# Optimization experiments

Measured on AMD Instinct MI355X. Metric: run time of the kernel, lower is better.

## Reference

```python
import jax, jax.numpy as jnp
import numpy as np

# SLAYER neuron / simulation parameters (from network.yaml)
THETA = 10.0      # spike threshold
TAU_SR = 10.0     # SRM (psp) kernel time constant
TAU_REF = 1.0     # refractory kernel time constant
SCALE_REF = 2.0   # refractory scale (kernel = -scaleRef*theta*alpha(t))
TS = 1.0          # simulation step (ms)
TK = 100          # FIR truncation length for the psp kernel (tauSr=10 -> fully decayed)

B, NIN, NHID, NOUT, T = 32, 2312, 512, 10, 350

# discrete refractory kernel ref[n] = C_REF * n * D_REF**n  (alpha shape)
D_REF = float(np.exp(-TS / TAU_REF))
C_REF = float(-SCALE_REF * THETA * np.e * TS / TAU_REF)


def srm_kernel():
    # eps(t) = (t/tauSr) * exp(1 - t/tauSr), peak value 1 at t = tauSr
    t = jnp.arange(TK, dtype=jnp.float32) * TS
    return (t / TAU_SR) * jnp.exp(1.0 - t / TAU_SR)


def psp(x):
    """Causal FIR filter along time. x: [B, C, T] -> [B, C, T]."""
    b, c, t = x.shape
    k = srm_kernel()[::-1].reshape(1, 1, TK)  # lax.conv correlates, so flip
    xp = jnp.pad(x.reshape(b * c, 1, t), ((0, 0), (0, 0), (TK - 1, 0)))
    y = jax.lax.conv_general_dilated(xp, k, (1,), 'VALID')
    return y.reshape(b, c, t)


def dense(W, x):
    # 1x1 conv over channels, applied at every time step
    return jnp.einsum('oi,bit->bot', W, x)


@jax.custom_vjp
def spike_fn(u):
    return (u >= THETA).astype(u.dtype)

def _spike_fwd(u):
    return spike_fn(u), u

def _spike_bwd(u, g):
    # SLAYER surrogate gradient: rho(u) = scaleRho * exp(-|u - theta| / tauRho)
    return (g * jnp.exp(-jnp.abs(u - THETA) / 1.0),)

spike_fn.defvjp(_spike_fwd, _spike_bwd)


def spike_layer(u_in):
    """Threshold-and-refractory spike dynamics via a 2-state IIR realization of
    the alpha refractory kernel. u_in: [B, C, T] -> spikes [B, C, T]."""
    uT = jnp.moveaxis(u_in, -1, 0)  # [T, B, C]
    zero = jnp.zeros(uT.shape[1:], uT.dtype)

    def step(carry, u_t):
        a, b = carry  # a = conv(spikes, D^n), b = conv(spikes, n*D^n)
        u = u_t + C_REF * b          # membrane = psp drive + refractory
        s = spike_fn(u)
        a_new = D_REF * a + s
        b_new = D_REF * b + D_REF * a
        return (a_new, b_new), s

    _, sT = jax.lax.scan(step, (zero, zero), uT)
    return jnp.moveaxis(sT, 0, -1)


def setup_inputs() -> dict:
    key = jax.random.key(0)
    k1, k2, k3 = jax.random.split(key, 3)
    spikeInput = (jax.random.uniform(k1, (B, NIN, T)) < 0.05).astype(jnp.float32)
    W1 = jax.random.normal(k2, (NHID, NIN), dtype=jnp.float32) * 0.05
    W2 = jax.random.normal(k3, (NOUT, NHID), dtype=jnp.float32) * 0.05
    return {"spikeInput": spikeInput, "W1": W1, "W2": W2}


def reference(spikeInput, W1, W2):
    s1 = spike_layer(dense(W1, psp(spikeInput)))
    s2 = spike_layer(dense(W2, psp(s1)))
    return s2
```

## Files before the change

kernel.cpp:

```cpp
#include <hip/hip_runtime.h>
#include <stdint.h>

#define B_SZ   32
#define NIN    2312
#define NHID   512
#define NOUT   10
#define T_SZ   350
#define NW32   73
#define NW64   8
#define NHALF  256
#define NROW   2313

#define DS_D   0.9048374180359595
#define CS_D   0.2718281828459045
#define D100_D 4.5399929762484854e-05
#define DREF_F 0.36787944117144233f
#define CREF_F -54.36563656918091f

#define NCHUNK 7
#define CLEN   50
#define NPF    10

__global__ __launch_bounds__(384) void k12(const float* __restrict__ x,
                                           const float* __restrict__ W1,
                                           uint32_t* __restrict__ bits1,
                                           float* __restrict__ W1s) {
    __shared__ float lds[32 * T_SZ];
    const int bid = blockIdx.x;
    const int tid = threadIdx.x;
    if (bid < NW32 * B_SZ) {
        const int w = bid % NW32;
        const int b = bid / NW32;
        const int rows = (NIN - (w << 5) < 32) ? (NIN - (w << 5)) : 32;
        const float* base = x + ((size_t)(b * NIN + (w << 5))) * T_SZ;
        const int nf4 = (rows * T_SZ) >> 2;
        for (int f = tid; f < nf4; f += 384)
            ((float4*)lds)[f] = ((const float4*)base)[f];
        __syncthreads();
        if (tid < T_SZ) {
            uint32_t bits = 0;
            for (int j = 0; j < rows; ++j)
                bits |= (lds[j * T_SZ + tid] > 0.5f) ? (1u << j) : 0u;
            bits1[(size_t)(b * T_SZ + tid) * NW32 + w] = bits;
        }
    } else if (bid < NW32 * B_SZ + NW32 * 16) {
        float (*tile)[33] = (float (*)[33])lds;
        const int bb = bid - NW32 * B_SZ;
        const int i0 = (bb % NW32) * 32, o0 = (bb / NW32) * 32;
        const int tx = tid & 31, ty = tid >> 5;
#pragma unroll
        for (int r = 0; r < 3; ++r) {
            int row = ty + 12 * r;
            if (row < 32) {
                int o = o0 + row, i = i0 + tx;
                if (i < NIN) tile[row][tx] = W1[(size_t)o * NIN + i];
            }
        }
        __syncthreads();
#pragma unroll
        for (int r = 0; r < 3; ++r) {
            int row = ty + 12 * r;
            if (row < 32) {
                int i = i0 + row, o = o0 + tx;
                if (i < NIN)
                    W1s[((size_t)(o >> 8) * NROW + i) * NHALF + (o & 255)] = tile[tx][row];
            }
        }
    } else {
        if (tid < NHALF) {
            W1s[((size_t)0 * NROW + NIN) * NHALF + tid] = 0.0f;
            W1s[((size_t)1 * NROW + NIN) * NHALF + tid] = 0.0f;
        }
    }
}

__global__ __launch_bounds__(256) void k3_dense1(const uint32_t* __restrict__ bits1,
                                                 const float* __restrict__ W1s,
                                                 float* __restrict__ z1ct) {
    __shared__ uint32_t words[128];
    __shared__ uint16_t pfx[80];
    __shared__ uint16_t idxbuf[NIN + 16];
    __shared__ float red[3][NHALF];
    __shared__ float fin[NHALF];

    const int id = blockIdx.x;
    const int h = (id >> 2) & 1;
    const int bt = ((id >> 3) << 2) | (id & 3);
    const int tid = threadIdx.x;
    const int wv = tid >> 6, lane = tid & 63;

    if (tid < 128) words[tid] = (tid < NW32) ? bits1[(size_t)bt * NW32 + tid] : 0u;
    __syncthreads();

    if (wv == 0) {
        uint32_t w0 = words[lane];
        uint32_t w1 = words[lane + 64];
        int p0 = __popc(w0), p1 = __popc(w1);
        int s0 = p0, s1 = p1;
#pragma unroll
        for (int off = 1; off < 64; off <<= 1) {
            int u0 = __shfl_up(s0, off);
            int u1 = __shfl_up(s1, off);
            if (lane >= off) { s0 += u0; s1 += u1; }
        }
        int tot0 = __shfl(s0, 63);
        pfx[lane] = (uint16_t)(s0 - p0);
        if (lane < 9) pfx[lane + 64] = (uint16_t)(tot0 + s1 - p1);
        if (lane == 8) pfx[73] = (uint16_t)(tot0 + s1);
    }
    __syncthreads();

    const int ntot = pfx[73];
    const int npad = (ntot + 15) & ~15;
    if (tid < NW32) {
        uint32_t m = words[tid];
        int p = pfx[tid];
        while (m) {
            int j = __builtin_ctz(m);
            m &= m - 1;
            idxbuf[p++] = (uint16_t)((tid << 5) + j);
        }
    }
    if (tid >= 240) {
        int k = tid - 240;
        if (ntot + k < npad) idxbuf[ntot + k] = (uint16_t)NIN;
    }
    __syncthreads();

    const float* Wh = W1s + (size_t)h * NROW * NHALF;
    float4 acc = make_float4(0.f, 0.f, 0.f, 0.f);
    for (int r = wv; r < npad; r += 16) {
        int i0 = idxbuf[r], i1 = idxbuf[r + 4], i2 = idxbuf[r + 8], i3 = idxbuf[r + 12];
        float4 v0 = ((const float4*)(Wh + (size_t)i0 * NHALF))[lane];
        float4 v1 = ((const float4*)(Wh + (size_t)i1 * NHALF))[lane];
        float4 v2 = ((const float4*)(Wh + (size_t)i2 * NHALF))[lane];
        float4 v3 = ((const float4*)(Wh + (size_t)i3 * NHALF))[lane];
        acc.x += v0.x; acc.y += v0.y; acc.z += v0.z; acc.w += v0.w;
        acc.x += v1.x; acc.y += v1.y; acc.z += v1.z; acc.w += v1.w;
        acc.x += v2.x; acc.y += v2.y; acc.z += v2.z; acc.w += v2.w;
        acc.x += v3.x; acc.y += v3.y; acc.z += v3.z; acc.w += v3.w;
    }
    if (wv > 0) ((float4*)red[wv - 1])[lane] = acc;
    __syncthreads();
    if (wv == 0) {
        float4 a1 = ((float4*)red[0])[lane];
        float4 a2 = ((float4*)red[1])[lane];
        float4 a3 = ((float4*)red[2])[lane];
        acc.x = ((acc.x + a1.x) + a2.x) + a3.x;
        acc.y = ((acc.y + a1.y) + a2.y) + a3.y;
        acc.z = ((acc.z + a1.z) + a2.z) + a3.z;
        acc.w = ((acc.w + a1.w) + a2.w) + a3.w;
        ((float4*)fin)[lane] = acc;
    }
    __syncthreads();
    const int och = (h << 8) + tid;
    const int oc = och >> 6, l6 = och & 63;
    const int b = bt / T_SZ, t = bt - b * T_SZ;
    z1ct[((size_t)(b * NW64 + oc) * T_SZ + t) * 64 + l6] = fin[tid];
}

__global__ __launch_bounds__(512) void k45(const float* __restrict__ z1ct,
                                           const float* __restrict__ W2,
                                           float* __restrict__ z2ct) {
    __shared__ float W2s[NHID * NOUT];
    __shared__ uint64_t sw[CLEN][NW64];
    const int tid = threadIdx.x;
    const int wv = tid >> 6, lane = tid & 63;
    const int b = blockIdx.x / NCHUNK;
    const int ck = blockIdx.x % NCHUNK;
    const int tstart = ck * CLEN;
    const int tend = tstart + CLEN;
    const int t0 = (tstart >= 100) ? tstart - 100 : 0;

    for (int k = tid; k < NHID * NOUT; k += 512) {
        int c = k / NOUT, o = k - c * NOUT;
        W2s[k] = W2[(size_t)o * NHID + c];
    }

    const float* base = z1ct + (size_t)(b * NW64 + wv) * T_SZ * 64 + lane;
    double A = 0.0, Bs = 0.0, A2 = 0.0, Bs2 = 0.0;
    float ra = 0.0f, rb = 0.0f;
    const double TAIL = D100_D * CS_D;
    float xb[NPF], xdb[NPF];
#pragma unroll
    for (int i = 0; i < NPF; ++i) {
        const int t = t0 + i;
        xb[i] = base[(size_t)t * 64];
        const int td = t - 100;
        const int tdc = (td >= 0) ? td : 0;
        float vd = base[(size_t)tdc * 64];
        xdb[i] = (td >= 0) ? vd : 0.0f;
    }
    for (int tb = t0; tb < tend; tb += NPF) {
        uint64_t mb[NPF];
#pragma unroll
        for (int i = 0; i < NPF; ++i) {
            const int t = tb + i;
            float x = xb[i], xd = xdb[i];
            const int tn = t + NPF;
            const int tcl = (tn < T_SZ) ? tn : (T_SZ - 1);
            float vb = base[(size_t)tcl * 64];
            xb[i] = (tn < T_SZ) ? vb : 0.0f;
            const int td = tn - 100;
            const int tdc = (td >= 0) ? td : 0;
            float vd = base[(size_t)tdc * 64];
            xdb[i] = (td >= 0) ? vd : 0.0f;
            Bs = DS_D * Bs + DS_D * A;
            A = DS_D * A + (double)x;
            Bs2 = DS_D * Bs2 + DS_D * A2;
            A2 = DS_D * A2 + (double)xd;
            double y = CS_D * Bs - TAIL * (Bs2 + 100.0 * A2);
            float u = (float)y + CREF_F * rb;
            float s = (u >= 10.0f) ? 1.0f : 0.0f;
            float ran = DREF_F * ra + s;
            float rbn = DREF_F * rb + DREF_F * ra;
            ra = ran; rb = rbn;
            mb[i] = __ballot(s != 0.0f);
        }
        if (tb >= tstart && lane == 0) {
#pragma unroll
            for (int i = 0; i < NPF; ++i)
                sw[tb - tstart + i][wv] = mb[i];
        }
    }
    __syncthreads();

    if (tid < CLEN * NOUT) {
        const int tr = tid / NOUT;
        const int o = tid - tr * NOUT;
        const int t = tstart + tr;
        float acc = 0.f;
#pragma unroll
        for (int w2 = 0; w2 < NW64; ++w2) {
            uint64_t m = sw[tr][w2];
            while (m) {
                int j = __builtin_ctzll(m);
                m &= m - 1;
                acc += W2s[((w2 << 6) + j) * NOUT + o];
            }
        }
        const int bo = b * NOUT + o;
        z2ct[((size_t)(bo >> 6) * T_SZ + t) * 64 + (bo & 63)] = acc;
    }
}

__global__ __launch_bounds__(64) void k6_fir_scan2(const float* __restrict__ z2ct,
                                                   float* __restrict__ out) {
    const int lane = threadIdx.x;
    const int g = blockIdx.x / NCHUNK;
    const int ck = blockIdx.x % NCHUNK;
    const int tstart = ck * CLEN;
    const int tend = tstart + CLEN;
    const int t0 = (tstart >= 100) ? tstart - 100 : 0;
    const int bo = (g << 6) + lane;
    const float* base = z2ct + (size_t)g * T_SZ * 64 + lane;
    float* op = out + (size_t)bo * T_SZ;
    double A = 0.0, Bs = 0.0, A2 = 0.0, Bs2 = 0.0;
    float ra = 0.0f, rb = 0.0f;
    const double TAIL = D100_D * CS_D;
    float xb[NPF], xdb[NPF];
#pragma unroll
    for (int i = 0; i < NPF; ++i) {
        const int t = t0 + i;
        xb[i] = base[(size_t)t * 64];
        const int td = t - 100;
        const int tdc = (td >= 0) ? td : 0;
        float vd = base[(size_t)tdc * 64];
        xdb[i] = (td >= 0) ? vd : 0.0f;
    }
    for (int tb = t0; tb < tend; tb += NPF) {
        float sb[NPF];
#pragma unroll
        for (int i = 0; i < NPF; ++i) {
            const int t = tb + i;
            float x = xb[i], xd = xdb[i];
            const int tn = t + NPF;
            const int tcl = (tn < T_SZ) ? tn : (T_SZ - 1);
            float vb = base[(size_t)tcl * 64];
            xb[i] = (tn < T_SZ) ? vb : 0.0f;
            const int td = tn - 100;
            const int tdc = (td >= 0) ? td : 0;
            float vd = base[(size_t)tdc * 64];
            xdb[i] = (td >= 0) ? vd : 0.0f;
            Bs = DS_D * Bs + DS_D * A;
            A = DS_D * A + (double)x;
            Bs2 = DS_D * Bs2 + DS_D * A2;
            A2 = DS_D * A2 + (double)xd;
            double y = CS_D * Bs - TAIL * (Bs2 + 100.0 * A2);
            float u = (float)y + CREF_F * rb;
            float s = (u >= 10.0f) ? 1.0f : 0.0f;
            float ran = DREF_F * ra + s;
            float rbn = DREF_F * rb + DREF_F * ra;
            ra = ran; rb = rbn;
            sb[i] = s;
        }
        if (tb >= tstart) {
#pragma unroll
            for (int i = 0; i < NPF; ++i)
                op[tb + i] = sb[i];
        }
    }
}

extern "C" void kernel_launch(void* const* d_in, const int* in_sizes, int n_in,
                              void* d_out, int out_size, void* d_ws, size_t ws_size,
                              hipStream_t stream) {
    const float* spikeInput = (const float*)d_in[0];
    const float* W1 = (const float*)d_in[1];
    const float* W2 = (const float*)d_in[2];
    float* out = (float*)d_out;

    char* ws = (char*)d_ws;
    float* W1s = (float*)(ws + 0);
    uint32_t* bits1 = (uint32_t*)(ws + 4737024);
    float* z1ct = (float*)(ws + 8007424);
    float* z2ct = (float*)(ws + 4737024);

    k12<<<NW32 * B_SZ + NW32 * 16 + 1, 384, 0, stream>>>(spikeInput, W1, bits1, W1s);
    k3_dense1<<<B_SZ * T_SZ * 2, 256, 0, stream>>>(bits1, W1s, z1ct);
    k45<<<B_SZ * NCHUNK, 512, 0, stream>>>(z1ct, W2, z2ct);
    k6_fir_scan2<<<5 * NCHUNK, 64, 0, stream>>>(z2ct, out);
}
```

Before: 295.9 us.

## Seed chunked FIR/IIR state with 4-way split warm-up instead of long burn-in

In the chunked time-parallel psp+spike kernels, each chunk other than the first previously replayed 100 steps of serial recurrence before its own 50 steps. Now it computes the IIR filter state at the chunk start directly, using four interleaved decimated accumulators (decay d^4) that are combined into the exact A/B states. A shorter 40-step serial burn-in is kept for the refractory spike state. This cuts the serial dependency chain per chunk, at the cost of extra loads and double-precision math. The shorter burn-in also risks refractory-state mismatch if spikes depend on history older than 40 steps.

```diff
diff --git a/kernel.cpp b/kernel.cpp
--- a/kernel.cpp
+++ b/kernel.cpp
@@ -12,6 +12,9 @@
 #define NROW   2313
 
 #define DS_D   0.9048374180359595
+#define DS2_D  0.8187307530779818
+#define DS3_D  0.7408182206817179
+#define DS4_D  0.6703200460356393
 #define CS_D   0.2718281828459045
 #define D100_D 4.5399929762484854e-05
 #define DREF_F 0.36787944117144233f
@@ -19,6 +22,7 @@
 
 #define NCHUNK 7
 #define CLEN   50
+#define BURN   40
 #define NPF    10
 
 __global__ __launch_bounds__(384) void k12(const float* __restrict__ x,
@@ -170,7 +174,7 @@
     const int ck = blockIdx.x % NCHUNK;
     const int tstart = ck * CLEN;
     const int tend = tstart + CLEN;
-    const int t0 = (tstart >= 100) ? tstart - 100 : 0;
+    const int t0 = (ck == 0) ? 0 : tstart - BURN;
 
     for (int k = tid; k < NHID * NOUT; k += 512) {
         int c = k / NOUT, o = k - c * NOUT;
@@ -181,6 +185,57 @@
     double A = 0.0, Bs = 0.0, A2 = 0.0, Bs2 = 0.0;
     float ra = 0.0f, rb = 0.0f;
     const double TAIL = D100_D * CS_D;
+
+    if (ck != 0) {
+        const int hi1 = t0 - 1;
+        const int hi2 = t0 - 101;
+        double F0=0,F1=0,F2=0,F3=0, G0=0,G1=0,G2=0,G3=0;
+        double P0=0,P1=0,P2=0,P3=0, Q0=0,Q1=0,Q2=0,Q3=0;
+#pragma unroll
+        for (int q = 0; q < 25; ++q) {
+            const int ta3 = hi1 - 99 + 4 * q;
+            const int c0 = (ta3     >= 0) ? ta3     : 0;
+            const int c1 = (ta3 + 1 >= 0) ? ta3 + 1 : 0;
+            const int c2 = (ta3 + 2 >= 0) ? ta3 + 2 : 0;
+            const int c3 = (ta3 + 3 >= 0) ? ta3 + 3 : 0;
+            float v0 = base[(size_t)c0 * 64];
+            float v1 = base[(size_t)c1 * 64];
+            float v2 = base[(size_t)c2 * 64];
+            float v3 = base[(size_t)c3 * 64];
+            float x3 = (ta3     >= 0) ? v0 : 0.f;
+            float x2 = (ta3 + 1 >= 0) ? v1 : 0.f;
+            float x1 = (ta3 + 2 >= 0) ? v2 : 0.f;
+            float x0 = (ta3 + 3 >= 0) ? v3 : 0.f;
+            G3 = DS4_D * G3 + DS4_D * F3; F3 = DS4_D * F3 + (double)x3;
+            G2 = DS4_D * G2 + DS4_D * F2; F2 = DS4_D * F2 + (double)x2;
+            G1 = DS4_D * G1 + DS4_D * F1; F1 = DS4_D * F1 + (double)x1;
+            G0 = DS4_D * G0 + DS4_D * F0; F0 = DS4_D * F0 + (double)x0;
+            const int tb3 = hi2 - 99 + 4 * q;
+            const int d0 = (tb3     >= 0) ? tb3     : 0;
+            const int d1 = (tb3 + 1 >= 0) ? tb3 + 1 : 0;
+            const int d2 = (tb3 + 2 >= 0) ? tb3 + 2 : 0;
+            const int d3 = (tb3 + 3 >= 0) ? tb3 + 3 : 0;
+            float w0 = base[(size_t)d0 * 64];
+            float w1 = base[(size_t)d1 * 64];
+            float w2 = base[(size_t)d2 * 64];
+            float w3 = base[(size_t)d3 * 64];
+            float y3 = (tb3     >= 0) ? w0 : 0.f;
+            float y2 = (tb3 + 1 >= 0) ? w1 : 0.f;
+            float y1 = (tb3 + 2 >= 0) ? w2 : 0.f;
+            float y0 = (tb3 + 3 >= 0) ? w3 : 0.f;
+            Q3 = DS4_D * Q3 + DS4_D * P3; P3 = DS4_D * P3 + (double)y3;
+            Q2 = DS4_D * Q2 + DS4_D * P2; P2 = DS4_D * P2 + (double)y2;
+            Q1 = DS4_D * Q1 + DS4_D * P1; P1 = DS4_D * P1 + (double)y1;
+            Q0 = DS4_D * Q0 + DS4_D * P0; P0 = DS4_D * P0 + (double)y0;
+        }
+        A   = F0 + DS_D * F1 + DS2_D * F2 + DS3_D * F3;
+        Bs  = 4.0 * G0 + DS_D * (F1 + 4.0 * G1)
+            + DS2_D * (2.0 * F2 + 4.0 * G2) + DS3_D * (3.0 * F3 + 4.0 * G3);
+        A2  = P0 + DS_D * P1 + DS2_D * P2 + DS3_D * P3;
+        Bs2 = 4.0 * Q0 + DS_D * (P1 + 4.0 * Q1)
+            + DS2_D * (2.0 * P2 + 4.0 * Q2) + DS3_D * (3.0 * P3 + 4.0 * Q3);
+    }
+
     float xb[NPF], xdb[NPF];
 #pragma unroll
     for (int i = 0; i < NPF; ++i) {
@@ -251,13 +306,64 @@
     const int ck = blockIdx.x % NCHUNK;
     const int tstart = ck * CLEN;
     const int tend = tstart + CLEN;
-    const int t0 = (tstart >= 100) ? tstart - 100 : 0;
+    const int t0 = (ck == 0) ? 0 : tstart - BURN;
     const int bo = (g << 6) + lane;
     const float* base = z2ct + (size_t)g * T_SZ * 64 + lane;
     float* op = out + (size_t)bo * T_SZ;
     double A = 0.0, Bs = 0.0, A2 = 0.0, Bs2 = 0.0;
     float ra = 0.0f, rb = 0.0f;
     const double TAIL = D100_D * CS_D;
+
+    if (ck != 0) {
+        const int hi1 = t0 - 1;
+        const int hi2 = t0 - 101;
+        double F0=0,F1=0,F2=0,F3=0, G0=0,G1=0,G2=0,G3=0;
+        double P0=0,P1=0,P2=0,P3=0, Q0=0,Q1=0,Q2=0,Q3=0;
+#pragma unroll
+        for (int q = 0; q < 25; ++q) {
+            const int ta3 = hi1 - 99 + 4 * q;
+            const int c0 = (ta3     >= 0) ? ta3     : 0;
+            const int c1 = (ta3 + 1 >= 0) ? ta3 + 1 : 0;
+            const int c2 = (ta3 + 2 >= 0) ? ta3 + 2 : 0;
+            const int c3 = (ta3 + 3 >= 0) ? ta3 + 3 : 0;
+            float v0 = base[(size_t)c0 * 64];
+            float v1 = base[(size_t)c1 * 64];
+            float v2 = base[(size_t)c2 * 64];
+            float v3 = base[(size_t)c3 * 64];
+            float x3 = (ta3     >= 0) ? v0 : 0.f;
+            float x2 = (ta3 + 1 >= 0) ? v1 : 0.f;
+            float x1 = (ta3 + 2 >= 0) ? v2 : 0.f;
+            float x0 = (ta3 + 3 >= 0) ? v3 : 0.f;
+            G3 = DS4_D * G3 + DS4_D * F3; F3 = DS4_D * F3 + (double)x3;
+            G2 = DS4_D * G2 + DS4_D * F2; F2 = DS4_D * F2 + (double)x2;
+            G1 = DS4_D * G1 + DS4_D * F1; F1 = DS4_D * F1 + (double)x1;
+            G0 = DS4_D * G0 + DS4_D * F0; F0 = DS4_D * F0 + (double)x0;
+            const int tb3 = hi2 - 99 + 4 * q;
+            const int d0 = (tb3     >= 0) ? tb3     : 0;
+            const int d1 = (tb3 + 1 >= 0) ? tb3 + 1 : 0;
+            const int d2 = (tb3 + 2 >= 0) ? tb3 + 2 : 0;
+            const int d3 = (tb3 + 3 >= 0) ? tb3 + 3 : 0;
+            float w0 = base[(size_t)d0 * 64];
+            float w1 = base[(size_t)d1 * 64];
+            float w2 = base[(size_t)d2 * 64];
+            float w3 = base[(size_t)d3 * 64];
+            float y3 = (tb3     >= 0) ? w0 : 0.f;
+            float y2 = (tb3 + 1 >= 0) ? w1 : 0.f;
+            float y1 = (tb3 + 2 >= 0) ? w2 : 0.f;
+            float y0 = (tb3 + 3 >= 0) ? w3 : 0.f;
+            Q3 = DS4_D * Q3 + DS4_D * P3; P3 = DS4_D * P3 + (double)y3;
+            Q2 = DS4_D * Q2 + DS4_D * P2; P2 = DS4_D * P2 + (double)y2;
+            Q1 = DS4_D * Q1 + DS4_D * P1; P1 = DS4_D * P1 + (double)y1;
+            Q0 = DS4_D * Q0 + DS4_D * P0; P0 = DS4_D * P0 + (double)y0;
+        }
+        A   = F0 + DS_D * F1 + DS2_D * F2 + DS3_D * F3;
+        Bs  = 4.0 * G0 + DS_D * (F1 + 4.0 * G1)
+            + DS2_D * (2.0 * F2 + 4.0 * G2) + DS3_D * (3.0 * F3 + 4.0 * G3);
+        A2  = P0 + DS_D * P1 + DS2_D * P2 + DS3_D * P3;
+        Bs2 = 4.0 * Q0 + DS_D * (P1 + 4.0 * Q1)
+            + DS2_D * (2.0 * P2 + 4.0 * Q2) + DS3_D * (3.0 * P3 + 4.0 * Q3);
+    }
+
     float xb[NPF], xdb[NPF];
 #pragma unroll
     for (int i = 0; i < NPF; ++i) {
```

Measured after the change: 311.2 us. +5.2%, slower.
